# Performance work log

Hardware: AMD Instinct MI355X
Metric: run time of the kernel (lower is better)

The kernel has to match this reference:

```python
import jax, jax.numpy as jnp
import numpy as np

B, N = 2, 6
C_IN, C_MID = 512, 512
D, C_OUT = 112, 80
OGH, OGW, DS = 256, 704, 16
FH, FW = OGH // DS, OGW // DS  # 16, 44
D_MIN, D_MAX = 2.0, 58.0
NX, NY, NZ = 128, 128, 1
VSIZE = np.array([0.8, 0.8, 8.0], dtype=np.float32)
VCOORD = np.array([-51.2 + 0.4, -51.2 + 0.4, -5.0 + 4.0], dtype=np.float32)


def make_frustum():
    # (D, FH, FW, 4) with entries (x_pix, y_pix, depth, 1)
    ones = jnp.ones((D, FH, FW), jnp.float32)
    d = jnp.linspace(D_MIN, D_MAX, D)[:, None, None] * jnp.ones((1, FH, FW))
    x = jnp.linspace(0.0, OGW - 1.0, FW)[None, None, :] * jnp.ones((D, FH, 1))
    y = jnp.linspace(0.0, OGH - 1.0, FH)[None, :, None] * jnp.ones((D, 1, FW))
    return jnp.stack([x, y, d, ones], axis=-1)


def setup_inputs() -> dict:
    key = jax.random.key(0)
    ks = jax.random.split(key, 24)
    eye = jnp.eye(4, dtype=jnp.float32)
    K = jnp.array([[1266.0, 0.0, 800.0, 0.0],
                   [0.0, 1266.0, 450.0, 0.0],
                   [0.0, 0.0, 1.0, 0.0],
                   [0.0, 0.0, 0.0, 1.0]], jnp.float32)
    inp = {
        'feat': jax.random.normal(ks[0], (B * N, C_IN, FH, FW), jnp.float32),
        'w1': 0.05 * jax.random.normal(ks[1], (C_MID, C_IN, 3, 3), jnp.float32),
        'g1': 1.0 + 0.1 * jax.random.normal(ks[2], (C_MID,), jnp.float32),
        'b1': 0.1 * jax.random.normal(ks[3], (C_MID,), jnp.float32),
        'm1': 0.1 * jax.random.normal(ks[4], (C_MID,), jnp.float32),
        'v1': 0.5 + jax.random.uniform(ks[5], (C_MID,), jnp.float32),
        'w2': 0.05 * jax.random.normal(ks[6], (C_MID, C_MID, 3, 3), jnp.float32),
        'g2': 1.0 + 0.1 * jax.random.normal(ks[7], (C_MID,), jnp.float32),
        'b2': 0.1 * jax.random.normal(ks[8], (C_MID,), jnp.float32),
        'm2': 0.1 * jax.random.normal(ks[9], (C_MID,), jnp.float32),
        'v2': 0.5 + jax.random.uniform(ks[10], (C_MID,), jnp.float32),
        'w_out': 0.05 * jax.random.normal(ks[11], (D + C_OUT, C_MID, 1, 1), jnp.float32),
        'b_out': 0.1 * jax.random.normal(ks[12], (D + C_OUT,), jnp.float32),
        'sensor2ego': eye + 0.05 * jax.random.normal(ks[13], (B, N, 4, 4), jnp.float32),
        'sensor2virtual': eye + 0.05 * jax.random.normal(ks[14], (B, N, 4, 4), jnp.float32),
        'intrin': K + 0.01 * jax.random.normal(ks[15], (B, N, 4, 4), jnp.float32),
        'ida': eye + 0.01 * jax.random.normal(ks[16], (B, N, 4, 4), jnp.float32),
        'ref_heights': 1.5 + 0.2 * jax.random.normal(ks[17], (B, N), jnp.float32),
        'bda': eye + 0.01 * jax.random.normal(ks[18], (B, 4, 4), jnp.float32),
    }
    return inp


def _conv(x, w, p):
    return jax.lax.conv_general_dilated(x, w, (1, 1), [(p, p), (p, p)],
                                         dimension_numbers=('NCHW', 'OIHW', 'NCHW'))


def _bn(x, g, b, m, v):
    s = (g / jnp.sqrt(v + 1e-5))
    return (x - m[None, :, None, None]) * s[None, :, None, None] + b[None, :, None, None]


def get_geometry(sensor2ego, sensor2virtual, intrin, ida, ref_heights, bda):
    frustum = make_frustum()[..., None]  # (D,FH,FW,4,1)
    pts = jnp.linalg.inv(ida)[:, :, None, None, None] @ frustum  # (B,N,D,FH,FW,4,1)
    ref = ref_heights[:, :, None, None, None, None]
    height = -pts[..., 2, :] + ref  # (B,N,D,FH,FW,1)
    pc = pts.at[..., 2, :].set(10.0)
    pc = jnp.concatenate([pc[..., :2, :] * pc[..., 2:3, :], pc[..., 2:, :]], axis=-2)
    cv = sensor2virtual @ jnp.linalg.inv(intrin)
    pv = cv[:, :, None, None, None] @ pc
    ratio = height[..., 0] / pv[..., 1, 0]  # (B,N,D,FH,FW)
    pts = pv * ratio[..., None, None]
    pts = pts.at[..., 3, :].set(1.0)
    ce = sensor2ego @ jnp.linalg.inv(sensor2virtual)
    pts = ce[:, :, None, None, None] @ pts
    pts = (bda[:, None, None, None, None] @ pts)[..., 0]
    return pts[..., :3]  # (B,N,D,FH,FW,3)


def reference(feat, w1, g1, b1, m1, v1, w2, g2, b2, m2, v2, w_out, b_out,
              sensor2ego, sensor2virtual, intrin, ida, ref_heights, bda):
    # DepthNet head
    h = jax.nn.relu(_bn(_conv(feat, w1, 1), g1, b1, m1, v1))
    h = jax.nn.relu(_bn(_conv(h, w2, 1), g2, b2, m2, v2))
    hf = _conv(h, w_out, 0) + b_out[None, :, None, None]  # (B*N, D+C, FH, FW)
    depth = jax.nn.softmax(hf[:, :D], axis=1).reshape(B, N, D, FH, FW)
    context = hf[:, D:].reshape(B, N, C_OUT, FH, FW)

    geom = get_geometry(sensor2ego, sensor2virtual, intrin, ida, ref_heights, bda)

    # voxel indices
    vsize = jnp.asarray(VSIZE)
    vcoord = jnp.asarray(VCOORD)
    idx = ((geom - (vcoord - vsize / 2.0)) / vsize).astype(jnp.int32)
    valid = (jnp.all(idx >= 0, axis=-1) & (idx[..., 0] < NX)
             & (idx[..., 1] < NY) & (idx[..., 2] < NZ))

    # LSS outer product: (B,N,D,FH,FW,C)
    vol = jnp.einsum('bndhw,bnchw->bndhwc', depth, context)
    YX = NY * NX
    sid = idx[..., 1] * NX + idx[..., 0] + jnp.arange(B, dtype=jnp.int32)[:, None, None, None, None] * YX
    sid = jnp.where(valid, sid, B * YX).reshape(-1)
    bev = jax.ops.segment_sum(vol.reshape(-1, C_OUT), sid, num_segments=B * YX + 1)[:B * YX]
    return bev.reshape(B, NY, NX, C_OUT).transpose(0, 3, 1, 2)  # (B,C,NY,NX)
```

## Files before the change

kernel.cpp:

```cpp
#include <hip/hip_runtime.h>
#include <stdint.h>

#define NB   2
#define NN   6
#define NIMG 12
#define CIN  512
#define CMID 512
#define DD   112
#define COUT 80
#define FHh  16
#define FWw  44
#define NPIX 704
#define NPOS 8448
#define KK   4608
#define NXg  128
#define NYg  128
#define YX   16384
#define MAT_STRIDE 56
#define PADPIX 828
#define PROW 46
#define KSPLIT 4
#define KCHUNK (KK/KSPLIT)
#define NSTEP (KCHUNK/32)

typedef short short8 __attribute__((ext_vector_type(8)));
typedef float f32x4  __attribute__((ext_vector_type(4)));

#define GLD16(g, l) __builtin_amdgcn_global_load_lds((const __attribute__((address_space(1))) void*)(g), (__attribute__((address_space(3))) void*)(l), 16, 0, 0)

__device__ __forceinline__ unsigned short f2bf(float f){
  unsigned u = __float_as_uint(f);
  u += 0x7fffu + ((u >> 16) & 1u);
  return (unsigned short)(u >> 16);
}
__device__ __forceinline__ float bf2f(unsigned short u){
  return __uint_as_float(((unsigned)u) << 16);
}

__device__ __forceinline__ f32x4 mfma16(short8 a, short8 b, f32x4 c){
  return __builtin_amdgcn_mfma_f32_16x16x32_bf16(a, b, c, 0, 0, 0);
}

#define N1 (CMID*KK)
__global__ void k_prep_misc(const float* __restrict__ w1, const float* __restrict__ w2,
                            const float* __restrict__ wout,
                            const float* __restrict__ g1, const float* __restrict__ b1,
                            const float* __restrict__ m1, const float* __restrict__ v1,
                            const float* __restrict__ g2, const float* __restrict__ b2,
                            const float* __restrict__ m2, const float* __restrict__ v2,
                            unsigned short* __restrict__ wb1, unsigned short* __restrict__ wb2,
                            unsigned short* __restrict__ wb3,
                            float* __restrict__ scale1, float* __restrict__ bias1,
                            float* __restrict__ scale2, float* __restrict__ bias2){
  int i = blockIdx.x*blockDim.x + threadIdx.x;
  if (i < 2*N1){
    const float* w = (i < N1) ? w1 : w2;
    unsigned short* wb = (i < N1) ? wb1 : wb2;
    int j = (i < N1) ? i : i - N1;
    int oc = j / KK; int jj = j - oc*KK;
    int r = jj >> 9; int ic = jj & 511;
    wb[j] = f2bf(w[(size_t)(oc*512 + ic)*9 + r]);
  } else if (i < 2*N1 + 192*CMID){
    int j = i - 2*N1;
    wb3[j] = f2bf(wout[j]);
  } else if (i < 2*N1 + 192*CMID + 512){
    int t = i - (2*N1 + 192*CMID);
    float s = g1[t] / sqrtf(v1[t] + 1e-5f);
    scale1[t] = s; bias1[t] = b1[t] - m1[t]*s;
  } else if (i < 2*N1 + 192*CMID + 1024){
    int t = i - (2*N1 + 192*CMID + 512);
    float s = g2[t] / sqrtf(v2[t] + 1e-5f);
    scale2[t] = s; bias2[t] = b2[t] - m2[t]*s;
  }
}

__global__ void k_zeropad(unsigned short* __restrict__ a, unsigned short* __restrict__ b,
                          float4* __restrict__ bev){
  int i = blockIdx.x*blockDim.x + threadIdx.x;
  if (i < NB*YX*COUT/4) bev[i] = make_float4(0.f,0.f,0.f,0.f);
  int img = i >> 16; int j = i & 65535;
  int seg = j >> 9, ch = j & 511;
  int pp;
  if (seg < 46)       pp = seg;
  else if (seg < 92)  pp = 17*PROW + (seg - 46);
  else { int s2 = seg - 92; int y = s2 >> 1; pp = y*PROW + ((s2 & 1) ? 45 : 0); }
  size_t off = (size_t)img*PADPIX*512 + (size_t)pp*512 + ch;
  a[off] = 0; b[off] = 0;
}

__global__ __launch_bounds__(256) void k_featpad(const float* __restrict__ feat,
                                                 unsigned short* __restrict__ dst){
  __shared__ float tile[32][65];
  int blk = blockIdx.x;
  int img = blk / 176; int r = blk - img*176;
  int cb = r / 11; int pb = r - cb*11;
  int c0 = cb*32, p0 = pb*64;
  int t = threadIdx.x;
  const float* s = feat + (size_t)img*CIN*NPIX + (size_t)c0*NPIX + p0;
  for (int ch = t>>6; ch < 32; ch += 4)
    tile[ch][t & 63] = s[(size_t)ch*NPIX + (t & 63)];
  __syncthreads();
  int ch = (t & 15)*2;
  for (int pix = t>>4; pix < 64; pix += 16){
    int p = p0 + pix;
    int y = p / FWw, x = p - y*FWw;
    unsigned v = (unsigned)f2bf(tile[ch][pix]) | ((unsigned)f2bf(tile[ch+1][pix]) << 16);
    *(unsigned*)(dst + (size_t)img*PADPIX*512 + ((y+1)*PROW + (x+1))*512 + c0 + ch) = v;
  }
}

__device__ void inv4(const double* A, double* out){
  double M[4][8];
  for (int i=0;i<4;i++){ for(int j=0;j<4;j++){ M[i][j]=A[i*4+j]; M[i][4+j]=(i==j)?1.0:0.0; } }
  for (int c=0;c<4;c++){
    int piv=c; double best=fabs(M[c][c]);
    for (int r=c+1;r<4;r++){ double a=fabs(M[r][c]); if(a>best){best=a;piv=r;} }
    if (piv!=c){ for(int j=0;j<8;j++){ double tt=M[c][j]; M[c][j]=M[piv][j]; M[piv][j]=tt; } }
    double inv = 1.0 / M[c][c];
    for (int j=0;j<8;j++) M[c][j]*=inv;
    for (int r=0;r<4;r++){ if(r==c) continue; double f=M[r][c];
      for (int j=0;j<8;j++) M[r][j]-=f*M[c][j]; }
  }
  for (int i=0;i<4;i++) for(int j=0;j<4;j++) out[i*4+j]=M[i][4+j];
}
__device__ void mm4(const double* A, const double* Bm, double* C){
  for (int i=0;i<4;i++) for(int j=0;j<4;j++){
    double s=0.0; for(int k=0;k<4;k++) s+=A[i*4+k]*Bm[k*4+j]; C[i*4+j]=s; }
}

__global__ void k_prep_mats(const float* __restrict__ s2e, const float* __restrict__ s2v,
                            const float* __restrict__ intr, const float* __restrict__ ida,
                            const float* __restrict__ refh, const float* __restrict__ bda,
                            double* __restrict__ mats){
  int t = threadIdx.x;
  if (t >= NIMG) return;
  int b = t / NN;
  double Mida[16], Ms2v[16], Mintr[16], Ms2e[16], Mbda[16];
  for (int i=0;i<16;i++){
    Mida[i] =(double)ida [t*16+i];
    Ms2v[i] =(double)s2v [t*16+i];
    Mintr[i]=(double)intr[t*16+i];
    Ms2e[i] =(double)s2e [t*16+i];
    Mbda[i] =(double)bda [b*16+i];
  }
  double* o = mats + (size_t)t*MAT_STRIDE;
  double tmp[16], tmp2[16];
  inv4(Mida, o);
  inv4(Mintr, tmp);  mm4(Ms2v, tmp, o+16);
  inv4(Ms2v, tmp);   mm4(Ms2e, tmp, tmp2);
  mm4(Mbda, tmp2, o+32);
  o[48] = (double)refh[t];
}

__global__ void k_geom(const double* __restrict__ mats, int* __restrict__ sid){
  int g = blockIdx.x*blockDim.x + threadIdx.x;
  int img = g / (DD*NPIX); int rem = g - img*(DD*NPIX);
  int d = rem / NPIX; int p = rem - d*NPIX;
  int h = p / FWw; int w = p - h*FWw;
  const double* M = mats + (size_t)img*MAT_STRIDE;
  float xf = (float)w * (703.0f/43.0f);
  float yf = (float)h * 17.0f;
  float df = 2.0f + (float)d * (56.0f/111.0f);
  double x = (double)xf, y = (double)yf, dep = (double)df;
  double p0 = M[0]*x + M[1]*y + M[2]*dep + M[3];
  double p1 = M[4]*x + M[5]*y + M[6]*dep + M[7];
  double p2 = M[8]*x + M[9]*y + M[10]*dep + M[11];
  double p3 = M[12]*x + M[13]*y + M[14]*dep + M[15];
  double height = M[48] - p2;
  double c0 = p0*10.0, c1 = p1*10.0, c2 = 10.0, c3 = p3;
  const double* C = M + 16;
  double q0 = C[0]*c0 + C[1]*c1 + C[2]*c2 + C[3]*c3;
  double q1 = C[4]*c0 + C[5]*c1 + C[6]*c2 + C[7]*c3;
  double q2 = C[8]*c0 + C[9]*c1 + C[10]*c2 + C[11]*c3;
  double ratio = height / q1;
  double r0 = q0*ratio, r1 = q1*ratio, r2 = q2*ratio, r3 = 1.0;
  const double* F = M + 32;
  double gx = F[0]*r0 + F[1]*r1 + F[2]*r2 + F[3]*r3;
  double gy = F[4]*r0 + F[5]*r1 + F[6]*r2 + F[7]*r3;
  double gz = F[8]*r0 + F[9]*r1 + F[10]*r2 + F[11]*r3;
  float gxf = (float)gx, gyf = (float)gy, gzf = (float)gz;
  const float vcx = (float)(-51.2 + 0.4);
  const float ox = vcx - 0.4f;
  const float oy = ox;
  const float oz = -1.0f - 4.0f;
  float tx = (gxf - ox) / 0.8f;
  float ty = (gyf - oy) / 0.8f;
  float tz = (gzf - oz) / 8.0f;
  int ix = (int)tx, iy = (int)ty, iz = (int)tz;
  bool valid = (tx==tx) && (ty==ty) && (tz==tz) &&
               (ix >= 0) && (ix < NXg) && (iy >= 0) && (iy < NYg) && (iz == 0);
  int b = img / NN;
  sid[g] = valid ? (b*YX + iy*NXg + ix) : -1;
}

__global__ __launch_bounds__(256, 4) void k_conv_sk(const unsigned short* __restrict__ W,
    const unsigned short* __restrict__ src, unsigned short* __restrict__ part){
  __shared__ __align__(16) short As[2][128*32];
  __shared__ __align__(16) short Bs[2][128*32];
  int t = threadIdx.x;
  int lane = t & 63, wv = t >> 6;
  int wm = wv >> 1, wn = wv & 1;
  int q = lane >> 4, ml = lane & 15;

  int id = blockIdx.x;
  int res = id & 7, slot = id >> 3;
  int g = res + 8*(slot >> 2);
  int mblk = slot & 3;
  int z = g / 66, n = g - z*66;
  int m0 = mblk*128, n0 = n*128, k0 = z*KCHUNK;

  int lrow = lane >> 2;
  int lcol = (lane & 3) * 8;
  const unsigned short* agp[2];
  const unsigned short* bgp[2];
  #pragma unroll
  for (int i=0;i<2;i++){
    int seg = wv*2 + i;
    agp[i] = W + (size_t)(m0 + seg*16 + lrow)*KK + lcol;
    int pos = n0 + seg*16 + lrow;
    int img = pos / NPIX; int p = pos - img*NPIX;
    int y = p / FWw; int x = p - y*FWw;
    bgp[i] = src + (size_t)img*PADPIX*512 + ((y+1)*PROW + (x+1))*512 + lcol;
  }

  f32x4 acc[4][4];
  #pragma unroll
  for (int i=0;i<4;i++)
    #pragma unroll
    for (int j=0;j<4;j++) acc[i][j] = (f32x4)0.0f;

  auto stage = [&](int step){
    int kb = k0 + step*32;
    int d = step & 1;
    int r = kb >> 9;
    int ic0 = kb & 511;
    int r3 = r / 3;
    int koff = (r3*PROW + (r - r3*3))*512 + ic0 - (PROW+1)*512;
    #pragma unroll
    for (int i=0;i<2;i++){
      int seg = wv*2 + i;
      GLD16(agp[i] + kb,   (char*)As[d] + seg*1024);
      GLD16(bgp[i] + koff, (char*)Bs[d] + seg*1024);
    }
  };

  stage(0);
  for (int k = 0; k < NSTEP; ++k){
    if (k + 1 < NSTEP){
      stage(k + 1);
      asm volatile("s_waitcnt vmcnt(4)" ::: "memory");
    } else {
      asm volatile("s_waitcnt vmcnt(0)" ::: "memory");
    }
    asm volatile("s_barrier" ::: "memory");
    const short* Ab = As[k & 1];
    const short* Bb = Bs[k & 1];
    short8 fa[4], fb[4];
    #pragma unroll
    for (int mi=0;mi<4;mi++) fa[mi] = *(const short8*)(Ab + (wm*64 + mi*16 + ml)*32 + q*8);
    #pragma unroll
    for (int ni=0;ni<4;ni++) fb[ni] = *(const short8*)(Bb + (wn*64 + ni*16 + ml)*32 + q*8);
    #pragma unroll
    for (int mi=0;mi<4;mi++)
      #pragma unroll
      for (int ni=0;ni<4;ni++)
        acc[mi][ni] = mfma16(fb[ni], fa[mi], acc[mi][ni]);
    asm volatile("s_barrier" ::: "memory");
  }

  unsigned short* op = part + (size_t)z*NPOS*CMID;
  #pragma unroll
  for (int mi=0;mi<4;mi++){
    int oc = m0 + wm*64 + mi*16 + ml;
    #pragma unroll
    for (int ni=0;ni<4;ni++){
      f32x4 v = acc[mi][ni];
      #pragma unroll
      for (int rr=0;rr<4;rr++){
        int pos = n0 + wn*64 + ni*16 + q*4 + rr;
        op[(size_t)pos*CMID + oc] = f2bf(v[rr]);
      }
    }
  }
}

template<int OUT_PADDED>
__global__ void k_reduce(const unsigned short* __restrict__ part,
                         const float* __restrict__ scale, const float* __restrict__ bias,
                         unsigned short* __restrict__ out){
  int i2 = blockIdx.x*blockDim.x + threadIdx.x;
  int e0 = i2*2;
  const size_t S = (size_t)NPOS*CMID;
  unsigned p0 = *(const unsigned*)(part + e0);
  unsigned p1 = *(const unsigned*)(part + e0 + S);
  unsigned p2 = *(const unsigned*)(part + e0 + 2*S);
  unsigned p3 = *(const unsigned*)(part + e0 + 3*S);
  float s0 = bf2f((unsigned short)p0) + bf2f((unsigned short)p1)
           + bf2f((unsigned short)p2) + bf2f((unsigned short)p3);
  float s1 = bf2f((unsigned short)(p0>>16)) + bf2f((unsigned short)(p1>>16))
           + bf2f((unsigned short)(p2>>16)) + bf2f((unsigned short)(p3>>16));
  int pos = e0 >> 9, oc = e0 & 511;
  float v0 = fmaxf(s0*scale[oc]   + bias[oc],   0.0f);
  float v1 = fmaxf(s1*scale[oc+1] + bias[oc+1], 0.0f);
  unsigned packed = (unsigned)f2bf(v0) | ((unsigned)f2bf(v1) << 16);
  if (OUT_PADDED){
    int img = pos / NPIX; int p = pos - img*NPIX;
    int y = p / FWw; int x = p - y*FWw;
    *(unsigned*)(out + (size_t)img*PADPIX*512 + ((y+1)*PROW + (x+1))*512 + oc) = packed;
  } else {
    *(unsigned*)(out + e0) = packed;
  }
}

__global__ __launch_bounds__(256) void k_gemm64(const unsigned short* __restrict__ A,
    const unsigned short* __restrict__ Bt, const float* __restrict__ bout,
    float* __restrict__ hf){
  const int K = 512;
  __shared__ __align__(16) short As[64][32];
  __shared__ __align__(16) short Bs[128][32];
  int t = threadIdx.x;
  int m0 = blockIdx.x*64; int n0 = blockIdx.y*128;
  int lane = t & 63; int wv = t >> 6; int q = lane >> 4, ml = lane & 15;
  f32x4 acc[8];
  #pragma unroll
  for (int i=0;i<8;i++) acc[i] = (f32x4)0.0f;
  int ar = t >> 2, ac = (t & 3) * 8;
  int br = t >> 1, bc = (t & 1) * 16;
  const unsigned short* pa = A  + (size_t)(m0 + ar)*K + ac;
  const unsigned short* pb = Bt + (size_t)(n0 + br)*K + bc;
  for (int kb = 0; kb < K; kb += 32){
    uint4 av = *(const uint4*)(pa + kb);
    uint4 b0 = *(const uint4*)(pb + kb);
    uint4 b1 = *(const uint4*)(pb + kb + 8);
    __syncthreads();
    *(uint4*)&As[ar][ac] = av;
    *(uint4*)&Bs[br][bc] = b0; *(uint4*)&Bs[br][bc+8] = b1;
    __syncthreads();
    short8 fa = *(const short8*)&As[wv*16 + ml][q*8];
    #pragma unroll
    for (int ni=0;ni<8;ni++){
      short8 fb = *(const short8*)&Bs[ni*16 + ml][q*8];
      acc[ni] = mfma16(fb, fa, acc[ni]);
    }
  }
  int oc = m0 + wv*16 + ml;
  float bb = bout[oc];
  #pragma unroll
  for (int ni=0;ni<8;ni++)
    #pragma unroll
    for (int r=0;r<4;r++){
      int pos = n0 + ni*16 + q*4 + r;
      hf[(size_t)pos*192 + oc] = acc[ni][r] + bb;
    }
}

__global__ void k_softmax(const float* __restrict__ hf, float* __restrict__ depth){
  int pos = blockIdx.x*4 + (threadIdx.x >> 6);
  int lane = threadIdx.x & 63;
  const float* row = hf + (size_t)pos*192;
  float v0 = row[lane];
  float v1 = (lane < DD-64) ? row[64 + lane] : -1e30f;
  float mx = fmaxf(v0, v1);
  #pragma unroll
  for (int m=1; m<64; m<<=1) mx = fmaxf(mx, __shfl_xor(mx, m, 64));
  float e0 = expf(v0 - mx);
  float e1 = (lane < DD-64) ? expf(v1 - mx) : 0.0f;
  float s = e0 + e1;
  #pragma unroll
  for (int m=1; m<64; m<<=1) s += __shfl_xor(s, m, 64);
  float inv = 1.0f / s;
  depth[(size_t)pos*DD + lane] = e0 * inv;
  if (lane < DD-64) depth[(size_t)pos*DD + 64 + lane] = e1 * inv;
}

__global__ void k_scatter(const float* __restrict__ depth, const float* __restrict__ hf,
                          const int* __restrict__ sidb, float* __restrict__ bev){
  int pos = blockIdx.x;
  int img = pos / NPIX; int p = pos - img*NPIX;
  __shared__ float sdep[DD];
  __shared__ int   ssid[DD];
  __shared__ float sctx[COUT];
  __shared__ float cwt[DD];
  __shared__ int   cvox[DD];
  __shared__ int   scnt;
  int t = threadIdx.x;
  if (t == 0) scnt = 0;
  if (t < DD){
    sdep[t] = depth[(size_t)pos*DD + t];
    ssid[t] = sidb[(size_t)(img*DD + t)*NPIX + p];
  }
  if (t < COUT) sctx[t] = hf[(size_t)pos*192 + DD + t];
  __syncthreads();
  if (t < DD){
    int s = ssid[t];
    bool head = (s >= 0) && (t == 0 || ssid[t-1] != s);
    if (head){
      float w = 0.0f;
      for (int dd = t; dd < DD && ssid[dd] == s; ++dd) w += sdep[dd];
      int i = atomicAdd(&scnt, 1);
      cvox[i] = s; cwt[i] = w;
    }
  }
  __syncthreads();
  int H = scnt;
  for (int j = t; j < H*COUT; j += 128){
    int h = j / COUT, c = j - h*COUT;
    atomicAdd(&bev[(size_t)cvox[h]*COUT + c], cwt[h]*sctx[c]);
  }
}

__global__ __launch_bounds__(256) void k_transpose(const float* __restrict__ bev, float* __restrict__ out){
  __shared__ float tile[64*COUT];
  int blk = blockIdx.x;
  int b = blk >> 8; int yx0 = (blk & 255) * 64;
  int t = threadIdx.x;
  const float* src = bev + ((size_t)b*YX + yx0)*COUT;
  for (int j = t; j < 64*COUT; j += 256) tile[j] = src[j];
  __syncthreads();
  float* dst = out + (size_t)b*COUT*YX + yx0;
  for (int j = t; j < COUT*64; j += 256){
    int c = j >> 6, row = j & 63;
    dst[(size_t)c*YX + row] = tile[row*COUT + c];
  }
}

extern "C" void kernel_launch(void* const* d_in, const int* in_sizes, int n_in,
                              void* d_out, int out_size, void* d_ws, size_t ws_size,
                              hipStream_t stream) {
  const float* feat = (const float*)d_in[0];
  const float* w1   = (const float*)d_in[1];
  const float* g1   = (const float*)d_in[2];
  const float* b1   = (const float*)d_in[3];
  const float* m1   = (const float*)d_in[4];
  const float* v1   = (const float*)d_in[5];
  const float* w2   = (const float*)d_in[6];
  const float* g2   = (const float*)d_in[7];
  const float* b2   = (const float*)d_in[8];
  const float* m2   = (const float*)d_in[9];
  const float* v2   = (const float*)d_in[10];
  const float* wout = (const float*)d_in[11];
  const float* bout = (const float*)d_in[12];
  const float* s2e  = (const float*)d_in[13];
  const float* s2v  = (const float*)d_in[14];
  const float* intr = (const float*)d_in[15];
  const float* ida  = (const float*)d_in[16];
  const float* refh = (const float*)d_in[17];
  const float* bda  = (const float*)d_in[18];

  uint8_t* base = (uint8_t*)d_ws;
  size_t off = 0;
  auto alloc = [&](size_t bytes)->void*{
    void* r = base + off;
    off = (off + bytes + 255) & ~(size_t)255;
    return r;
  };
  unsigned short* wb1 = (unsigned short*)alloc((size_t)CMID*KK*2);
  unsigned short* wb2 = (unsigned short*)alloc((size_t)CMID*KK*2);
  unsigned short* wb3 = (unsigned short*)alloc((size_t)192*CMID*2);
  float* scale1 = (float*)alloc(CMID*4);
  float* bias1  = (float*)alloc(CMID*4);
  float* scale2 = (float*)alloc(CMID*4);
  float* bias2  = (float*)alloc(CMID*4);
  double* mats  = (double*)alloc((size_t)NIMG*MAT_STRIDE*8);

  size_t padded_bytes = (size_t)NIMG*PADPIX*512*2;
  uint8_t* regionE = (uint8_t*)alloc(padded_bytes);
  uint8_t* regionF = (uint8_t*)alloc(padded_bytes);
  float* depth = (float*)alloc((size_t)NPOS*DD*4);
  int*   sid   = (int*)  alloc((size_t)NIMG*DD*NPIX*4);
  float* bev   = (float*)alloc((size_t)NB*YX*COUT*4);
  unsigned short* part = (unsigned short*)alloc((size_t)KSPLIT*NPOS*CMID*2);

  unsigned short* featpad = (unsigned short*)regionE;
  unsigned short* h2      = (unsigned short*)regionE;
  unsigned short* h1pad   = (unsigned short*)regionF;
  float*          hf      = (float*)regionF;

  int prep_n = 2*N1 + 192*CMID + 1024;
  k_prep_misc<<<(prep_n + 255)/256, 256, 0, stream>>>(w1, w2, wout, g1, b1, m1, v1,
      g2, b2, m2, v2, wb1, wb2, wb3, scale1, bias1, scale2, bias2);
  k_prep_mats<<<1, 64, 0, stream>>>(s2e, s2v, intr, ida, refh, bda, mats);
  k_geom<<<3696, 256, 0, stream>>>(mats, sid);

  k_zeropad<<<3072, 256, 0, stream>>>(featpad, h1pad, (float4*)bev);
  k_featpad<<<2112, 256, 0, stream>>>(feat, featpad);

  k_conv_sk<<<1056, 256, 0, stream>>>(wb1, featpad, part);
  k_reduce<1><<<NPOS*CMID/512, 256, 0, stream>>>(part, scale1, bias1, h1pad);
  k_conv_sk<<<1056, 256, 0, stream>>>(wb2, h1pad, part);
  k_reduce<0><<<NPOS*CMID/512, 256, 0, stream>>>(part, scale2, bias2, h2);
  k_gemm64<<<dim3(3, 66), 256, 0, stream>>>(wb3, h2, bout, hf);

  k_softmax<<<2112, 256, 0, stream>>>(hf, depth);

  k_scatter<<<NPOS, 128, 0, stream>>>(depth, hf, sid, bev);

  k_transpose<<<512, 256, 0, stream>>>(bev, (float*)d_out);
}
```

Baseline: 371.1 us.

## Triple-buffer conv LDS pipeline and fuse depth softmax into scatter kernel

```diff
diff --git a/kernel.cpp b/kernel.cpp
--- a/kernel.cpp
+++ b/kernel.cpp
@@ -195,8 +195,8 @@
 
 __global__ __launch_bounds__(256, 4) void k_conv_sk(const unsigned short* __restrict__ W,
     const unsigned short* __restrict__ src, unsigned short* __restrict__ part){
-  __shared__ __align__(16) short As[2][128*32];
-  __shared__ __align__(16) short Bs[2][128*32];
+  __shared__ __align__(16) short As[3][128*32];
+  __shared__ __align__(16) short Bs[3][128*32];
   int t = threadIdx.x;
   int lane = t & 63, wv = t >> 6;
   int wm = wv >> 1, wn = wv & 1;
@@ -229,9 +229,8 @@
     #pragma unroll
     for (int j=0;j<4;j++) acc[i][j] = (f32x4)0.0f;
 
-  auto stage = [&](int step){
+  auto stage = [&](int step, int d){
     int kb = k0 + step*32;
-    int d = step & 1;
     int r = kb >> 9;
     int ic0 = kb & 511;
     int r3 = r / 3;
@@ -244,17 +243,18 @@
     }
   };
 
-  stage(0);
+  stage(0, 0); stage(1, 1);
+  int d = 0;
   for (int k = 0; k < NSTEP; ++k){
-    if (k + 1 < NSTEP){
-      stage(k + 1);
-      asm volatile("s_waitcnt vmcnt(4)" ::: "memory");
-    } else {
-      asm volatile("s_waitcnt vmcnt(0)" ::: "memory");
-    }
+    if (k < NSTEP-1) asm volatile("s_waitcnt vmcnt(4)" ::: "memory");
+    else             asm volatile("s_waitcnt vmcnt(0)" ::: "memory");
     asm volatile("s_barrier" ::: "memory");
-    const short* Ab = As[k & 1];
-    const short* Bb = Bs[k & 1];
+    if (k + 2 < NSTEP){
+      int nxt = d + 2; if (nxt >= 3) nxt -= 3;
+      stage(k + 2, nxt);
+    }
+    const short* Ab = As[d];
+    const short* Bb = Bs[d];
     short8 fa[4], fb[4];
     #pragma unroll
     for (int mi=0;mi<4;mi++) fa[mi] = *(const short8*)(Ab + (wm*64 + mi*16 + ml)*32 + q*8);
@@ -265,7 +265,7 @@
       #pragma unroll
       for (int ni=0;ni<4;ni++)
         acc[mi][ni] = mfma16(fb[ni], fa[mi], acc[mi][ni]);
-    asm volatile("s_barrier" ::: "memory");
+    d = (d == 2) ? 0 : d + 1;
   }
 
   unsigned short* op = part + (size_t)z*NPOS*CMID;
@@ -354,26 +354,7 @@
     }
 }
 
-__global__ void k_softmax(const float* __restrict__ hf, float* __restrict__ depth){
-  int pos = blockIdx.x*4 + (threadIdx.x >> 6);
-  int lane = threadIdx.x & 63;
-  const float* row = hf + (size_t)pos*192;
-  float v0 = row[lane];
-  float v1 = (lane < DD-64) ? row[64 + lane] : -1e30f;
-  float mx = fmaxf(v0, v1);
-  #pragma unroll
-  for (int m=1; m<64; m<<=1) mx = fmaxf(mx, __shfl_xor(mx, m, 64));
-  float e0 = expf(v0 - mx);
-  float e1 = (lane < DD-64) ? expf(v1 - mx) : 0.0f;
-  float s = e0 + e1;
-  #pragma unroll
-  for (int m=1; m<64; m<<=1) s += __shfl_xor(s, m, 64);
-  float inv = 1.0f / s;
-  depth[(size_t)pos*DD + lane] = e0 * inv;
-  if (lane < DD-64) depth[(size_t)pos*DD + 64 + lane] = e1 * inv;
-}
-
-__global__ void k_scatter(const float* __restrict__ depth, const float* __restrict__ hf,
+__global__ __launch_bounds__(128) void k_scatter(const float* __restrict__ hf,
                           const int* __restrict__ sidb, float* __restrict__ bev){
   int pos = blockIdx.x;
   int img = pos / NPIX; int p = pos - img*NPIX;
@@ -383,22 +364,38 @@
   __shared__ float cwt[DD];
   __shared__ int   cvox[DD];
   __shared__ int   scnt;
-  int t = threadIdx.x;
+  __shared__ float redm[2];
+  __shared__ float reds[2];
+  int t = threadIdx.x;
+  int wv = t >> 6;
   if (t == 0) scnt = 0;
+  const float* row = hf + (size_t)pos*192;
+  float v = (t < DD) ? row[t] : -1e30f;
+  for (int c = t; c < COUT; c += 128) sctx[c] = row[DD + c];
+  if (t < DD) ssid[t] = sidb[(size_t)(img*DD + t)*NPIX + p];
+  float m = v;
+  #pragma unroll
+  for (int o=32;o>=1;o>>=1) m = fmaxf(m, __shfl_xor(m, o, 64));
+  if ((t & 63) == 0) redm[wv] = m;
+  __syncthreads();
+  float mx = fmaxf(redm[0], redm[1]);
+  float e = (t < DD) ? __expf(v - mx) : 0.0f;
+  float s = e;
+  #pragma unroll
+  for (int o=32;o>=1;o>>=1) s += __shfl_xor(s, o, 64);
+  if ((t & 63) == 0) reds[wv] = s;
+  __syncthreads();
+  float inv = 1.0f / (reds[0] + reds[1]);
+  if (t < DD) sdep[t] = e * inv;
+  __syncthreads();
   if (t < DD){
-    sdep[t] = depth[(size_t)pos*DD + t];
-    ssid[t] = sidb[(size_t)(img*DD + t)*NPIX + p];
-  }
-  if (t < COUT) sctx[t] = hf[(size_t)pos*192 + DD + t];
-  __syncthreads();
-  if (t < DD){
-    int s = ssid[t];
-    bool head = (s >= 0) && (t == 0 || ssid[t-1] != s);
+    int sd = ssid[t];
+    bool head = (sd >= 0) && (t == 0 || ssid[t-1] != sd);
     if (head){
       float w = 0.0f;
-      for (int dd = t; dd < DD && ssid[dd] == s; ++dd) w += sdep[dd];
+      for (int dd = t; dd < DD && ssid[dd] == sd; ++dd) w += sdep[dd];
       int i = atomicAdd(&scnt, 1);
-      cvox[i] = s; cwt[i] = w;
+      cvox[i] = sd; cwt[i] = w;
     }
   }
   __syncthreads();
@@ -466,7 +463,6 @@
   size_t padded_bytes = (size_t)NIMG*PADPIX*512*2;
   uint8_t* regionE = (uint8_t*)alloc(padded_bytes);
   uint8_t* regionF = (uint8_t*)alloc(padded_bytes);
-  float* depth = (float*)alloc((size_t)NPOS*DD*4);
   int*   sid   = (int*)  alloc((size_t)NIMG*DD*NPIX*4);
   float* bev   = (float*)alloc((size_t)NB*YX*COUT*4);
   unsigned short* part = (unsigned short*)alloc((size_t)KSPLIT*NPOS*CMID*2);
@@ -491,9 +487,7 @@
   k_reduce<0><<<NPOS*CMID/512, 256, 0, stream>>>(part, scale2, bias2, h2);
   k_gemm64<<<dim3(3, 66), 256, 0, stream>>>(wb3, h2, bout, hf);
 
-  k_softmax<<<2112, 256, 0, stream>>>(hf, depth);
-
-  k_scatter<<<NPOS, 128, 0, stream>>>(depth, hf, sid, bev);
+  k_scatter<<<NPOS, 128, 0, stream>>>(hf, sid, bev);
 
   k_transpose<<<512, 256, 0, stream>>>(bev, (float*)d_out);
 }
```

New measurement: 372.2 us. No clear change (+0.3%).
